# Kernel tuning notes

Hardware: AMD Instinct MI355X
Metric: run time of the kernel (lower is better)

The kernel has to match this reference:

```python
import jax, jax.numpy as jnp
import numpy as np

G, B, S, D = 4, 1, 1024, 2048   # num_gpus (chunks), batch, seq_local, model dim
H, DH = 32, 64                  # heads, dim_head; inner_dim = H*DH = D
EPS = 1e-6
NEG = -1e30                     # finite stand-in for -inf lse init (grad-safe)


def setup_inputs() -> dict:
    key = jax.random.key(0)
    ks = jax.random.split(key, 8)
    wsc = 1.0 / np.sqrt(D)  # keep pre-softmax logits in a sane range
    return {
        'x':  jax.random.normal(ks[0], (G, B, S, D), jnp.float32),
        'Wq': jax.random.normal(ks[1], (D, D), jnp.float32) * wsc,
        'bq': jnp.zeros((D,), jnp.float32),
        'Wk': jax.random.normal(ks[2], (D, D), jnp.float32) * wsc,
        'bk': jnp.zeros((D,), jnp.float32),
        'Wv': jax.random.normal(ks[3], (D, D), jnp.float32) * wsc,
        'bv': jnp.zeros((D,), jnp.float32),
        'qn_w': jnp.ones((D,), jnp.float32),
        'kn_w': jnp.ones((D,), jnp.float32),
        'Wo': jax.random.normal(ks[4], (D, D), jnp.float32) * wsc,
        'bo': jnp.zeros((D,), jnp.float32),
    }


def _rms_norm(t, w):
    return t * jax.lax.rsqrt(jnp.mean(t * t, axis=-1, keepdims=True) + EPS) * w


def reference(x, Wq, bq, Wk, bk, Wv, bv, qn_w, kn_w, Wo, bo):
    # x: [G, B, S, D] -- per-'GPU' sequence chunks
    q = _rms_norm(x @ Wq.T + bq, qn_w)
    k = _rms_norm(x @ Wk.T + bk, kn_w)
    v = x @ Wv.T + bv
    split = lambda t: t.reshape(G, B, S, H, DH).transpose(0, 1, 3, 2, 4)  # [G,B,H,S,DH]
    q, k, v = split(q), split(k), split(v)
    scale = 1.0 / np.sqrt(DH)

    out = jnp.zeros_like(q)
    lse = jnp.full((G, B, H, S, 1), NEG, q.dtype)
    kc, vc = k, v
    # Ring: each chunk attends to the visiting K/V chunk with online softmax.
    for _ in range(G):
        scores = jnp.einsum('gbhqd,gbhkd->gbhqk', q, kc) * scale
        m = scores.max(axis=-1, keepdims=True)
        e = jnp.exp(scores - m)
        ssum = e.sum(axis=-1, keepdims=True)
        chunk_lse = m + jnp.log(ssum)
        chunk_out = jnp.einsum('gbhqk,gbhkd->gbhqd', e / ssum, vc)
        new_lse = jnp.logaddexp(lse, chunk_lse)
        out = out * jnp.exp(lse - new_lse) + chunk_out * jnp.exp(chunk_lse - new_lse)
        lse = new_lse
        # rotate K/V around the ring: device i receives from device i-1
        kc = jnp.roll(kc, 1, axis=0)
        vc = jnp.roll(vc, 1, axis=0)

    o = out.transpose(0, 1, 3, 2, 4).reshape(G, B, S, H * DH)
    return o @ Wo.T + bo
```

## Files before the change

### kernel.cpp

```cpp
#include <hip/hip_runtime.h>

typedef __bf16 bf16x8 __attribute__((ext_vector_type(8)));
typedef float f32x4 __attribute__((ext_vector_type(4)));
typedef float f32x16 __attribute__((ext_vector_type(16)));
typedef unsigned short u16x8 __attribute__((ext_vector_type(8)));
typedef unsigned u32x2 __attribute__((ext_vector_type(2)));
typedef unsigned u32x4 __attribute__((ext_vector_type(4)));

__device__ __forceinline__ unsigned short f2bf(float f) {
  union { float f; unsigned u; } v; v.f = f;
  unsigned r = (v.u + 0x7fffu + ((v.u >> 16) & 1u)) >> 16;
  return (unsigned short)r;
}
__device__ __forceinline__ float bf2f(unsigned short s) {
  union { unsigned u; float f; } v; v.u = ((unsigned)s) << 16;
  return v.f;
}

#define GLD16(g, l)                                                        \
  __builtin_amdgcn_global_load_lds(                                        \
      (const __attribute__((address_space(1))) void*)(g),                  \
      (__attribute__((address_space(3))) void*)(l), 16, 0, 0)

__device__ __forceinline__ int swzc(int row, int colel) {
  return colel ^ ((((row & 7) ^ ((row >> 3) & 7)) & 7) << 3);
}

__device__ __forceinline__ u32x2 plswap(unsigned a, unsigned b) {
  return __builtin_amdgcn_permlane32_swap(a, b, false, false);
}
__device__ __forceinline__ float pair_sum(float x) {
  u32x2 r = plswap(__float_as_uint(x), __float_as_uint(x));
  return __uint_as_float(r.x) + __uint_as_float(r.y);
}
__device__ __forceinline__ unsigned cvtpk(float a, float b) {
  unsigned r;
  asm("v_cvt_pk_bf16_f32 %0, %1, %2" : "=v"(r) : "v"(a), "v"(b));
  return r;
}

__global__ __launch_bounds__(256) void cast_all_kernel(
    const float* __restrict__ x,
    const float* __restrict__ w0, const float* __restrict__ w1,
    const float* __restrict__ w2, const float* __restrict__ w3,
    unsigned short* __restrict__ xo,
    unsigned short* __restrict__ o0, unsigned short* __restrict__ o1,
    unsigned short* __restrict__ o2, unsigned short* __restrict__ o3) {
  int i = blockIdx.x * 256 + threadIdx.x;
  int stride = gridDim.x * 256;
  for (; i < 6291456; i += stride) {
    const float* src;
    unsigned short* dst;
    int j;
    if (i < 2097152) {
      src = x; dst = xo; j = i;
    } else {
      int k = i - 2097152;
      int sel = k >> 20;
      src = sel == 0 ? w0 : sel == 1 ? w1 : sel == 2 ? w2 : w3;
      dst = sel == 0 ? o0 : sel == 1 ? o1 : sel == 2 ? o2 : o3;
      j = k & 1048575;
    }
    float4 f = reinterpret_cast<const float4*>(src)[j];
    ushort4 s;
    s.x = f2bf(f.x); s.y = f2bf(f.y); s.z = f2bf(f.z); s.w = f2bf(f.w);
    reinterpret_cast<ushort4*>(dst)[j] = s;
  }
}


#define SGA(SLICE, SLOT)                                                       \
  GLD16(Ag + (size_t)(row0 + ar0) * 2048 + (SLICE) * 32 + ac0,                 \
        &As[SLOT][ci0 * 512]);                                                 \
  GLD16(Ag + (size_t)(row0 + ar1) * 2048 + (SLICE) * 32 + ac1,                 \
        &As[SLOT][ci1 * 512]);

#define SGB(SLICE, SLOT)                                                       \
  GLD16(Bg + (size_t)(col0 + br0) * 2048 + (SLICE) * 32 + bc0,                 \
        &Bs[SLOT][wid * 512]);

#define VM3 asm volatile("s_waitcnt vmcnt(3)" ::: "memory");
#define VM0 asm volatile("s_waitcnt vmcnt(0)" ::: "memory");

#define PH256(SLOT, STG, VMW)                                                  \
  {                                                                            \
    bf16x8 a0 = *(const bf16x8*)&As[SLOT][offA[0]];                            \
    bf16x8 a1 = *(const bf16x8*)&As[SLOT][offA[1]];                            \
    bf16x8 a2 = *(const bf16x8*)&As[SLOT][offA[2]];                            \
    bf16x8 a3 = *(const bf16x8*)&As[SLOT][offA[3]];                            \
    bf16x8 b0 = *(const bf16x8*)&Bs[SLOT][offB[0]];                            \
    bf16x8 b1 = *(const bf16x8*)&Bs[SLOT][offB[1]];                            \
    bf16x8 b2 = *(const bf16x8*)&Bs[SLOT][offB[2]];                            \
    bf16x8 b3 = *(const bf16x8*)&Bs[SLOT][offB[3]];                            \
    STG;                                                                       \
    __builtin_amdgcn_s_barrier();                                              \
    __builtin_amdgcn_s_setprio(1);                                             \
    acc[0][0] = __builtin_amdgcn_mfma_f32_16x16x32_bf16(a0, b0, acc[0][0], 0, 0, 0); \
    acc[0][1] = __builtin_amdgcn_mfma_f32_16x16x32_bf16(a0, b1, acc[0][1], 0, 0, 0); \
    acc[0][2] = __builtin_amdgcn_mfma_f32_16x16x32_bf16(a0, b2, acc[0][2], 0, 0, 0); \
    acc[0][3] = __builtin_amdgcn_mfma_f32_16x16x32_bf16(a0, b3, acc[0][3], 0, 0, 0); \
    acc[1][0] = __builtin_amdgcn_mfma_f32_16x16x32_bf16(a1, b0, acc[1][0], 0, 0, 0); \
    acc[1][1] = __builtin_amdgcn_mfma_f32_16x16x32_bf16(a1, b1, acc[1][1], 0, 0, 0); \
    acc[1][2] = __builtin_amdgcn_mfma_f32_16x16x32_bf16(a1, b2, acc[1][2], 0, 0, 0); \
    acc[1][3] = __builtin_amdgcn_mfma_f32_16x16x32_bf16(a1, b3, acc[1][3], 0, 0, 0); \
    acc[2][0] = __builtin_amdgcn_mfma_f32_16x16x32_bf16(a2, b0, acc[2][0], 0, 0, 0); \
    acc[2][1] = __builtin_amdgcn_mfma_f32_16x16x32_bf16(a2, b1, acc[2][1], 0, 0, 0); \
    acc[2][2] = __builtin_amdgcn_mfma_f32_16x16x32_bf16(a2, b2, acc[2][2], 0, 0, 0); \
    acc[2][3] = __builtin_amdgcn_mfma_f32_16x16x32_bf16(a2, b3, acc[2][3], 0, 0, 0); \
    acc[3][0] = __builtin_amdgcn_mfma_f32_16x16x32_bf16(a3, b0, acc[3][0], 0, 0, 0); \
    acc[3][1] = __builtin_amdgcn_mfma_f32_16x16x32_bf16(a3, b1, acc[3][1], 0, 0, 0); \
    acc[3][2] = __builtin_amdgcn_mfma_f32_16x16x32_bf16(a3, b2, acc[3][2], 0, 0, 0); \
    acc[3][3] = __builtin_amdgcn_mfma_f32_16x16x32_bf16(a3, b3, acc[3][3], 0, 0, 0); \
    __builtin_amdgcn_s_setprio(0);                                             \
    VMW;                                                                       \
    __builtin_amdgcn_s_barrier();                                              \
  }

template <int F32OUT>
__global__ __launch_bounds__(512, 4) void gemm256(
    const unsigned short* __restrict__ Ag,
    const unsigned short* __restrict__ W0, const unsigned short* __restrict__ W1,
    const unsigned short* __restrict__ W2,
    const float* __restrict__ b0, const float* __restrict__ b1,
    const float* __restrict__ b2,
    void* __restrict__ C0, void* __restrict__ C1, void* __restrict__ C2) {
  __shared__ unsigned short As[3][8192];
  __shared__ unsigned short Bs[3][4096];

  const int lin = blockIdx.y * gridDim.x + blockIdx.x;
  const int cpx = (gridDim.x * gridDim.y) >> 3;
  const int swz = (lin & 7) * cpx + (lin >> 3);
  const int bx = swz % gridDim.x, by = swz / gridDim.x;

  const int gcol = bx * 128;
  const int sel = gcol >> 11;
  const unsigned short* Bg = sel == 0 ? W0 : sel == 1 ? W1 : W2;
  const float* bias = sel == 0 ? b0 : sel == 1 ? b1 : b2;
  void* Cp = sel == 0 ? C0 : sel == 1 ? C1 : C2;
  const int col0 = gcol & 2047;
  const int row0 = by * 256;

  const int tid = threadIdx.x, lane = tid & 63, wid = tid >> 6;
  const int l15 = lane & 15, l4 = lane >> 4;
  const int wm = wid >> 1, wn = wid & 1;

  const int sl2a = ((lane >> 2) & 3) ^ ((lane >> 4) & 3);
  const int ci0 = wid * 2, ci1 = wid * 2 + 1;
  const int ar0 = ci0 * 16 + (lane >> 2);
  const int ar1 = ci1 * 16 + (lane >> 2);
  const int ac0 = (((lane & 3) ^ sl2a ^ (ci0 & 3)) & 3) * 8;
  const int ac1 = (((lane & 3) ^ sl2a ^ (ci1 & 3)) & 3) * 8;
  const int br0 = wid * 16 + (lane >> 2);
  const int bc0 = (((lane & 3) ^ sl2a ^ (wid & 3)) & 3) * 8;

  const int lsel = (l15 & 3) ^ ((l15 >> 2) & 3);
  int offA[4], offB[4];
#pragma unroll
  for (int f = 0; f < 4; ++f)
    offA[f] = (wm * 64 + f * 16 + l15) * 32 + ((l4 ^ lsel ^ f) & 3) * 8;
#pragma unroll
  for (int ni = 0; ni < 4; ++ni)
    offB[ni] = (wn * 64 + ni * 16 + l15) * 32 + ((l4 ^ lsel ^ ni) & 3) * 8;

  f32x4 acc[4][4] = {};

  SGA(0, 0); SGB(0, 0);
  SGA(1, 1); SGB(1, 1);
  VM3;
  __builtin_amdgcn_s_barrier();

  for (int it = 0; it < 20; ++it) {
    const int s = 3 * it;
    PH256(0, SGA(s + 2, 2) SGB(s + 2, 2), VM3);
    PH256(1, SGA(s + 3, 0) SGB(s + 3, 0), VM3);
    PH256(2, SGA(s + 4, 1) SGB(s + 4, 1), VM3);
  }
  PH256(0, SGA(62, 2) SGB(62, 2), VM3);
  PH256(1, SGA(63, 0) SGB(63, 0), VM3);
  PH256(2, , VM0);
  PH256(0, , );

#pragma unroll
  for (int f = 0; f < 4; ++f)
#pragma unroll
    for (int ni = 0; ni < 4; ++ni)
#pragma unroll
      for (int r = 0; r < 4; ++r) {
        int row = row0 + wm * 64 + f * 16 + l4 * 4 + r;
        int col = col0 + wn * 64 + ni * 16 + l15;
        float v = acc[f][ni][r] + bias[col];
        if (F32OUT)
          ((float*)Cp)[(size_t)row * 2048 + col] = v;
        else
          ((unsigned short*)Cp)[(size_t)row * 2048 + col] = f2bf(v);
      }
}

__global__ __launch_bounds__(256) void rmsnorm2_kernel(
    unsigned short* __restrict__ Qb, unsigned short* __restrict__ Kb,
    const float* __restrict__ qw, const float* __restrict__ kw) {
  const int row = blockIdx.x;
  unsigned short* p;
  const float* w;
  if (row < 4096) { p = Qb + (size_t)row * 2048; w = qw; }
  else            { p = Kb + (size_t)(row - 4096) * 2048; w = kw; }
  const int tid = threadIdx.x;
  u16x8 v = *(const u16x8*)&p[tid * 8];
  float f[8];
  float ss = 0.f;
#pragma unroll
  for (int j = 0; j < 8; ++j) { f[j] = bf2f(v[j]); ss += f[j] * f[j]; }
#pragma unroll
  for (int m = 1; m < 64; m <<= 1) ss += __shfl_xor(ss, m, 64);
  __shared__ float red[4];
  const int wid = tid >> 6, lane = tid & 63;
  if (lane == 0) red[wid] = ss;
  __syncthreads();
  float tot = red[0] + red[1] + red[2] + red[3];
  float rs = rsqrtf(tot * (1.0f / 2048.0f) + 1e-6f);
  u16x8 o;
#pragma unroll
  for (int j = 0; j < 8; ++j) o[j] = f2bf(f[j] * rs * w[tid * 8 + j]);
  *(u16x8*)&p[tid * 8] = o;
}

__global__ __launch_bounds__(256, 2) void flash_attn(
    const unsigned short* __restrict__ Q, const unsigned short* __restrict__ K,
    const unsigned short* __restrict__ V, unsigned short* __restrict__ O) {
  __shared__ unsigned short Ks[2][64 * 64];
  __shared__ unsigned short Vs[2][64 * 64];
  const int bid = blockIdx.x;
  const int sw = (bid & 7) * 64 + (bid >> 3);
  const int h = sw >> 4;
  const int q0 = (sw & 15) * 256;
  const int tid = threadIdx.x, lane = tid & 63, wid = tid >> 6;
  const int l31 = lane & 31, hi = lane >> 5;

  const int kr0 = wid * 16 + (lane >> 3);
  const int kc0 = (lane & 7) * 8;
  const int vkey = (tid & 31) * 2;
  const int vd0 = (tid >> 5) * 8;

  const float QSCALE = 0.125f * 1.44269504f;
  bf16x8 qf0[4], qf1[4];
  {
    const int qr0 = q0 + wid * 64 + l31;
#pragma unroll
    for (int kt = 0; kt < 4; ++kt) {
      bf16x8 r0 = *(const bf16x8*)&Q[(size_t)qr0 * 2048 + h * 64 + kt * 16 + hi * 8];
      bf16x8 r1 = *(const bf16x8*)&Q[(size_t)(qr0 + 32) * 2048 + h * 64 + kt * 16 + hi * 8];
#pragma unroll
      for (int j = 0; j < 8; ++j) {
        qf0[kt][j] = (__bf16)((float)r0[j] * QSCALE);
        qf1[kt][j] = (__bf16)((float)r1[j] * QSCALE);
      }
    }
  }

  int off[2][4];
#pragma unroll
  for (int kb = 0; kb < 2; ++kb) {
    const int row = kb * 32 + l31;
    const int sl = (((row & 7) ^ ((row >> 3) & 7)) & 7) << 3;
#pragma unroll
    for (int kt = 0; kt < 4; ++kt)
      off[kb][kt] = row * 64 + ((kt * 16 + hi * 8) ^ sl);
  }

  float l0 = 0.f, l1 = 0.f;
  f32x16 oa0[2] = {}, oa1[2] = {};

  u16x8 kreg0, kreg1, vreg0, vreg1;
  auto loadKV = [&](int kt0) {
    kreg0 = *(const u16x8*)&K[(size_t)(kt0 + kr0) * 2048 + h * 64 + kc0];
    kreg1 = *(const u16x8*)&K[(size_t)(kt0 + kr0 + 8) * 2048 + h * 64 + kc0];
    vreg0 = *(const u16x8*)&V[(size_t)(kt0 + vkey) * 2048 + h * 64 + vd0];
    vreg1 = *(const u16x8*)&V[(size_t)(kt0 + vkey + 1) * 2048 + h * 64 + vd0];
  };
  auto writeKV = [&](int b) {
    *(u16x8*)&Ks[b][kr0 * 64 + swzc(kr0, kc0)] = kreg0;
    *(u16x8*)&Ks[b][(kr0 + 8) * 64 + swzc(kr0 + 8, kc0)] = kreg1;
#pragma unroll
    for (int d = 0; d < 8; ++d) {
      int row = vd0 + d;
      *(unsigned*)&Vs[b][row * 64 + swzc(row, vkey)] =
          (unsigned)vreg0[d] | ((unsigned)vreg1[d] << 16);
    }
  };

  loadKV(0);
  writeKV(0);
  __syncthreads();

  for (int t = 0; t < 64; ++t) {
    const int cur = t & 1;
    if (t < 63) loadKV((t + 1) * 64);

    const unsigned short* Kc = Ks[cur];
    const unsigned short* Vc = Vs[cur];

    bf16x8 kf[2][4];
#pragma unroll
    for (int kb = 0; kb < 2; ++kb)
#pragma unroll
      for (int kt = 0; kt < 4; ++kt)
        kf[kb][kt] = *(const bf16x8*)&Kc[off[kb][kt]];

    f32x16 st0[2], st1[2];
    __builtin_amdgcn_s_setprio(1);
#pragma unroll
    for (int kb = 0; kb < 2; ++kb) {
      f32x16 a = {};
#pragma unroll
      for (int kt = 0; kt < 4; ++kt)
        a = __builtin_amdgcn_mfma_f32_32x32x16_bf16(kf[kb][kt], qf0[kt], a, 0, 0, 0);
      st0[kb] = a;
    }
#pragma unroll
    for (int kb = 0; kb < 2; ++kb) {
      f32x16 a = {};
#pragma unroll
      for (int kt = 0; kt < 4; ++kt)
        a = __builtin_amdgcn_mfma_f32_32x32x16_bf16(kf[kb][kt], qf1[kt], a, 0, 0, 0);
      st1[kb] = a;
    }
    __builtin_amdgcn_s_setprio(0);

    unsigned pk0[16], pk1[16];
    {
      float s0 = 0.f, s1 = 0.f, s2 = 0.f, s3 = 0.f;
#pragma unroll
      for (int kb = 0; kb < 2; ++kb)
#pragma unroll
        for (int j = 0; j < 8; ++j) {
          float pa = __builtin_amdgcn_exp2f(st0[kb][2 * j]);
          float pb = __builtin_amdgcn_exp2f(st0[kb][2 * j + 1]);
          if ((j & 3) == 0) s0 += pa + pb;
          else if ((j & 3) == 1) s1 += pa + pb;
          else if ((j & 3) == 2) s2 += pa + pb;
          else s3 += pa + pb;
          pk0[kb * 8 + j] = cvtpk(pa, pb);
        }
      l0 += (s0 + s1) + (s2 + s3);
    }
    {
      float s0 = 0.f, s1 = 0.f, s2 = 0.f, s3 = 0.f;
#pragma unroll
      for (int kb = 0; kb < 2; ++kb)
#pragma unroll
        for (int j = 0; j < 8; ++j) {
          float pa = __builtin_amdgcn_exp2f(st1[kb][2 * j]);
          float pb = __builtin_amdgcn_exp2f(st1[kb][2 * j + 1]);
          if ((j & 3) == 0) s0 += pa + pb;
          else if ((j & 3) == 1) s1 += pa + pb;
          else if ((j & 3) == 2) s2 += pa + pb;
          else s3 += pa + pb;
          pk1[kb * 8 + j] = cvtpk(pa, pb);
        }
      l1 += (s0 + s1) + (s2 + s3);
    }

    bf16x8 pfrag0[4], pfrag1[4];
#pragma unroll
    for (int kt = 0; kt < 4; ++kt) {
      u32x2 sa = plswap(pk0[4 * kt + 0], pk0[4 * kt + 2]);
      u32x2 sb = plswap(pk0[4 * kt + 1], pk0[4 * kt + 3]);
      union { u32x4 u; bf16x8 b; } w;
      w.u.x = sa.x; w.u.y = sb.x; w.u.z = sa.y; w.u.w = sb.y;
      pfrag0[kt] = w.b;
      u32x2 sc = plswap(pk1[4 * kt + 0], pk1[4 * kt + 2]);
      u32x2 sd = plswap(pk1[4 * kt + 1], pk1[4 * kt + 3]);
      union { u32x4 u; bf16x8 b; } w2;
      w2.u.x = sc.x; w2.u.y = sd.x; w2.u.z = sc.y; w2.u.w = sd.y;
      pfrag1[kt] = w2.b;
    }

    __builtin_amdgcn_s_setprio(1);
#pragma unroll
    for (int dv = 0; dv < 2; ++dv) {
      bf16x8 vf[4];
#pragma unroll
      for (int kt = 0; kt < 4; ++kt)
        vf[kt] = *(const bf16x8*)&Vc[off[dv][kt]];
#pragma unroll
      for (int kt = 0; kt < 4; ++kt)
        oa0[dv] = __builtin_amdgcn_mfma_f32_32x32x16_bf16(vf[kt], pfrag0[kt], oa0[dv], 0, 0, 0);
#pragma unroll
      for (int kt = 0; kt < 4; ++kt)
        oa1[dv] = __builtin_amdgcn_mfma_f32_32x32x16_bf16(vf[kt], pfrag1[kt], oa1[dv], 0, 0, 0);
    }
    __builtin_amdgcn_s_setprio(0);

    if (t < 63) {
      writeKV(cur ^ 1);
      __syncthreads();
    }
  }

  const float inv0 = 1.0f / pair_sum(l0);
  const float inv1 = 1.0f / pair_sum(l1);
  const int qr0 = q0 + wid * 64 + l31;
#pragma unroll
  for (int dv = 0; dv < 2; ++dv)
#pragma unroll
    for (int tq = 0; tq < 4; ++tq) {
      int dh = 32 * dv + 8 * tq + 4 * hi;
      unsigned a0 = cvtpk(oa0[dv][4 * tq + 0] * inv0, oa0[dv][4 * tq + 1] * inv0);
      unsigned a1 = cvtpk(oa0[dv][4 * tq + 2] * inv0, oa0[dv][4 * tq + 3] * inv0);
      u32x2 wa = {a0, a1};
      *(u32x2*)&O[(size_t)qr0 * 2048 + h * 64 + dh] = wa;
      unsigned b0 = cvtpk(oa1[dv][4 * tq + 0] * inv1, oa1[dv][4 * tq + 1] * inv1);
      unsigned b1 = cvtpk(oa1[dv][4 * tq + 2] * inv1, oa1[dv][4 * tq + 3] * inv1);
      u32x2 wb = {b0, b1};
      *(u32x2*)&O[(size_t)(qr0 + 32) * 2048 + h * 64 + dh] = wb;
    }
}

extern "C" void kernel_launch(void* const* d_in, const int* in_sizes, int n_in,
                              void* d_out, int out_size, void* d_ws, size_t ws_size,
                              hipStream_t stream) {
  const float* x  = (const float*)d_in[0];
  const float* Wq = (const float*)d_in[1];
  const float* bq = (const float*)d_in[2];
  const float* Wk = (const float*)d_in[3];
  const float* bk = (const float*)d_in[4];
  const float* Wv = (const float*)d_in[5];
  const float* bv = (const float*)d_in[6];
  const float* qn = (const float*)d_in[7];
  const float* kn = (const float*)d_in[8];
  const float* Wo = (const float*)d_in[9];
  const float* bo = (const float*)d_in[10];

  char* w = (char*)d_ws;
  unsigned short* Xbf = (unsigned short*)(w);
  unsigned short* Wqb = (unsigned short*)(w + 16777216);
  unsigned short* Wkb = (unsigned short*)(w + 25165824);
  unsigned short* Wvb = (unsigned short*)(w + 33554432);
  unsigned short* Wob = (unsigned short*)(w + 41943040);
  unsigned short* Qb  = (unsigned short*)(w + 50331648);
  unsigned short* Kb  = (unsigned short*)(w + 67108864);
  unsigned short* Vb  = (unsigned short*)(w + 83886080);
  unsigned short* Ob  = Xbf;

  cast_all_kernel<<<3072, 256, 0, stream>>>(x, Wq, Wk, Wv, Wo,
                                            Xbf, Wqb, Wkb, Wvb, Wob);

  gemm256<0><<<dim3(48, 16), 512, 0, stream>>>(
      Xbf, Wqb, Wkb, Wvb, bq, bk, bv, Qb, Kb, Vb);

  rmsnorm2_kernel<<<8192, 256, 0, stream>>>(Qb, Kb, qn, kn);

  flash_attn<<<512, 256, 0, stream>>>(Qb, Kb, Vb, Ob);

  gemm256<1><<<dim3(16, 16), 512, 0, stream>>>(
      Ob, Wob, Wob, Wob, bo, bo, bo, d_out, d_out, d_out);
}
```

Before: 361.0 us.

## Use 256x256 tile GEMM for fused QKV projection

Adds a new gemm512 kernel with a 256x256 output tile (8 waves, each computing 128x64) for the fused QKV projection, replacing the 256x128 tile kernel. Larger tiles raise arithmetic intensity and halve B-operand refetches per output, cutting global/L2 traffic. In exchange it doubles LDS per block and uses more accumulator registers, lowering occupancy to 2 blocks per CU, and the grid shrinks to 384 blocks. The output projection is specialized into a non-templated f32 kernel.

```diff
diff --git a/kernel.cpp b/kernel.cpp
--- a/kernel.cpp
+++ b/kernel.cpp
@@ -69,6 +69,114 @@
 }
 
 
+#define SG2A(SLICE, SLOT)                                                      \
+  GLD16(Ag + (size_t)(row0 + ar0) * 2048 + (SLICE) * 32 + ac0,                 \
+        &As2[SLOT][ci0 * 512]);                                                \
+  GLD16(Ag + (size_t)(row0 + ar1) * 2048 + (SLICE) * 32 + ac1,                 \
+        &As2[SLOT][ci1 * 512]);
+
+#define SG2B(SLICE, SLOT)                                                      \
+  GLD16(Bg + (size_t)(col0 + ar0) * 2048 + (SLICE) * 32 + ac0,                 \
+        &Bs2[SLOT][ci0 * 512]);                                                \
+  GLD16(Bg + (size_t)(col0 + ar1) * 2048 + (SLICE) * 32 + ac1,                 \
+        &Bs2[SLOT][ci1 * 512]);
+
+#define VM4 asm volatile("s_waitcnt vmcnt(4)" ::: "memory");
+#define VM0 asm volatile("s_waitcnt vmcnt(0)" ::: "memory");
+
+#define PH512(SLOT, STG, VMW)                                                  \
+  {                                                                            \
+    bf16x8 af[8], bb[4];                                                       \
+    _Pragma("unroll") for (int f = 0; f < 8; ++f)                              \
+        af[f] = *(const bf16x8*)&As2[SLOT][offA[f]];                           \
+    _Pragma("unroll") for (int n = 0; n < 4; ++n)                              \
+        bb[n] = *(const bf16x8*)&Bs2[SLOT][offB[n]];                           \
+    STG;                                                                       \
+    __builtin_amdgcn_s_barrier();                                              \
+    __builtin_amdgcn_s_setprio(1);                                             \
+    _Pragma("unroll") for (int f = 0; f < 8; ++f)                              \
+      _Pragma("unroll") for (int n = 0; n < 4; ++n)                            \
+        acc[f][n] = __builtin_amdgcn_mfma_f32_16x16x32_bf16(                   \
+            af[f], bb[n], acc[f][n], 0, 0, 0);                                 \
+    __builtin_amdgcn_s_setprio(0);                                             \
+    VMW;                                                                       \
+    __builtin_amdgcn_s_barrier();                                              \
+  }
+
+__global__ __launch_bounds__(512, 2) void gemm512(
+    const unsigned short* __restrict__ Ag,
+    const unsigned short* __restrict__ W0, const unsigned short* __restrict__ W1,
+    const unsigned short* __restrict__ W2,
+    const float* __restrict__ b0, const float* __restrict__ b1,
+    const float* __restrict__ b2,
+    unsigned short* __restrict__ C0, unsigned short* __restrict__ C1,
+    unsigned short* __restrict__ C2) {
+  __shared__ unsigned short As2[3][8192];
+  __shared__ unsigned short Bs2[3][8192];
+
+  const int lin = blockIdx.y * gridDim.x + blockIdx.x;
+  const int cpx = (gridDim.x * gridDim.y) >> 3;
+  const int swz = (lin & 7) * cpx + (lin >> 3);
+  const int bx = swz % gridDim.x, by = swz / gridDim.x;
+
+  const int gcol = bx * 256;
+  const int sel = gcol >> 11;
+  const unsigned short* Bg = sel == 0 ? W0 : sel == 1 ? W1 : W2;
+  const float* bias = sel == 0 ? b0 : sel == 1 ? b1 : b2;
+  unsigned short* Cp = sel == 0 ? C0 : sel == 1 ? C1 : C2;
+  const int col0 = gcol & 2047;
+  const int row0 = by * 256;
+
+  const int tid = threadIdx.x, lane = tid & 63, wid = tid >> 6;
+  const int l15 = lane & 15, l4 = lane >> 4;
+  const int wm = wid >> 2, wn = wid & 3;
+
+  const int sl2a = ((lane >> 2) & 3) ^ ((lane >> 4) & 3);
+  const int ci0 = wid * 2, ci1 = wid * 2 + 1;
+  const int ar0 = ci0 * 16 + (lane >> 2);
+  const int ar1 = ci1 * 16 + (lane >> 2);
+  const int ac0 = (((lane & 3) ^ sl2a ^ (ci0 & 3)) & 3) * 8;
+  const int ac1 = (((lane & 3) ^ sl2a ^ (ci1 & 3)) & 3) * 8;
+
+  const int lsel = (l15 & 3) ^ ((l15 >> 2) & 3);
+  int offA[8], offB[4];
+#pragma unroll
+  for (int f = 0; f < 8; ++f)
+    offA[f] = (wm * 128 + f * 16 + l15) * 32 + ((l4 ^ lsel ^ (f & 3)) & 3) * 8;
+#pragma unroll
+  for (int n = 0; n < 4; ++n)
+    offB[n] = (wn * 64 + n * 16 + l15) * 32 + ((l4 ^ lsel ^ (n & 3)) & 3) * 8;
+
+  f32x4 acc[8][4] = {};
+
+  SG2A(0, 0); SG2B(0, 0);
+  SG2A(1, 1); SG2B(1, 1);
+  VM4;
+  __builtin_amdgcn_s_barrier();
+
+  for (int it = 0; it < 20; ++it) {
+    const int s = 3 * it;
+    PH512(0, SG2A(s + 2, 2) SG2B(s + 2, 2), VM4);
+    PH512(1, SG2A(s + 3, 0) SG2B(s + 3, 0), VM4);
+    PH512(2, SG2A(s + 4, 1) SG2B(s + 4, 1), VM4);
+  }
+  PH512(0, SG2A(62, 2) SG2B(62, 2), VM4);
+  PH512(1, SG2A(63, 0) SG2B(63, 0), VM4);
+  PH512(2, , VM0);
+  PH512(0, , );
+
+#pragma unroll
+  for (int f = 0; f < 8; ++f)
+#pragma unroll
+    for (int ni = 0; ni < 4; ++ni)
+#pragma unroll
+      for (int r = 0; r < 4; ++r) {
+        int row = row0 + wm * 128 + f * 16 + l4 * 4 + r;
+        int col = col0 + wn * 64 + ni * 16 + l15;
+        Cp[(size_t)row * 2048 + col] = f2bf(acc[f][ni][r] + bias[col]);
+      }
+}
+
 #define SGA(SLICE, SLOT)                                                       \
   GLD16(Ag + (size_t)(row0 + ar0) * 2048 + (SLICE) * 32 + ac0,                 \
         &As[SLOT][ci0 * 512]);                                                 \
@@ -80,7 +188,6 @@
         &Bs[SLOT][wid * 512]);
 
 #define VM3 asm volatile("s_waitcnt vmcnt(3)" ::: "memory");
-#define VM0 asm volatile("s_waitcnt vmcnt(0)" ::: "memory");
 
 #define PH256(SLOT, STG, VMW)                                                  \
   {                                                                            \
@@ -116,14 +223,9 @@
     __builtin_amdgcn_s_barrier();                                              \
   }
 
-template <int F32OUT>
-__global__ __launch_bounds__(512, 4) void gemm256(
-    const unsigned short* __restrict__ Ag,
-    const unsigned short* __restrict__ W0, const unsigned short* __restrict__ W1,
-    const unsigned short* __restrict__ W2,
-    const float* __restrict__ b0, const float* __restrict__ b1,
-    const float* __restrict__ b2,
-    void* __restrict__ C0, void* __restrict__ C1, void* __restrict__ C2) {
+__global__ __launch_bounds__(512, 4) void gemm256_f32(
+    const unsigned short* __restrict__ Ag, const unsigned short* __restrict__ Bg,
+    const float* __restrict__ bias, float* __restrict__ Cp) {
   __shared__ unsigned short As[3][8192];
   __shared__ unsigned short Bs[3][4096];
 
@@ -132,12 +234,7 @@
   const int swz = (lin & 7) * cpx + (lin >> 3);
   const int bx = swz % gridDim.x, by = swz / gridDim.x;
 
-  const int gcol = bx * 128;
-  const int sel = gcol >> 11;
-  const unsigned short* Bg = sel == 0 ? W0 : sel == 1 ? W1 : W2;
-  const float* bias = sel == 0 ? b0 : sel == 1 ? b1 : b2;
-  void* Cp = sel == 0 ? C0 : sel == 1 ? C1 : C2;
-  const int col0 = gcol & 2047;
+  const int col0 = bx * 128;
   const int row0 = by * 256;
 
   const int tid = threadIdx.x, lane = tid & 63, wid = tid >> 6;
@@ -188,11 +285,7 @@
       for (int r = 0; r < 4; ++r) {
         int row = row0 + wm * 64 + f * 16 + l4 * 4 + r;
         int col = col0 + wn * 64 + ni * 16 + l15;
-        float v = acc[f][ni][r] + bias[col];
-        if (F32OUT)
-          ((float*)Cp)[(size_t)row * 2048 + col] = v;
-        else
-          ((unsigned short*)Cp)[(size_t)row * 2048 + col] = f2bf(v);
+        Cp[(size_t)row * 2048 + col] = acc[f][ni][r] + bias[col];
       }
 }
 
@@ -445,13 +538,12 @@
   cast_all_kernel<<<3072, 256, 0, stream>>>(x, Wq, Wk, Wv, Wo,
                                             Xbf, Wqb, Wkb, Wvb, Wob);
 
-  gemm256<0><<<dim3(48, 16), 512, 0, stream>>>(
+  gemm512<<<dim3(24, 16), 512, 0, stream>>>(
       Xbf, Wqb, Wkb, Wvb, bq, bk, bv, Qb, Kb, Vb);
 
   rmsnorm2_kernel<<<8192, 256, 0, stream>>>(Qb, Kb, qn, kn);
 
   flash_attn<<<512, 256, 0, stream>>>(Qb, Kb, Vb, Ob);
 
-  gemm256<1><<<dim3(16, 16), 512, 0, stream>>>(
-      Ob, Wob, Wob, Wob, bo, bo, bo, d_out, d_out, d_out);
-}
+  gemm256_f32<<<dim3(16, 16), 512, 0, stream>>>(Ob, Wob, bo, (float*)d_out);
+}
```

Result: no change. 366.9 us (+1.6%).
